# Kernel tuning notes

Hardware: AMD Instinct MI355X
Metric: run time of the kernel (lower is better)

The kernel has to match this reference:

```python
import jax, jax.numpy as jnp
import numpy as np

B, T = 2048, 256
VOCAB, E, H = 50000, 50, 50


def setup_inputs() -> dict:
    key = jax.random.key(0)
    ks = jax.random.split(key, 9)
    s = 0.1
    return {
        "batched_input": jax.random.randint(ks[0], (B, T), 0, VOCAB),
        "emb": jax.random.normal(ks[1], (VOCAB, E)) * s,
        "Wk": jax.random.normal(ks[2], (E, 4 * H)) * s,      # LSTM input kernel (i,f,c,o)
        "Uk": jax.random.normal(ks[3], (H, 4 * H)) * s,      # LSTM recurrent kernel
        "b": jnp.zeros((4 * H,)),                            # LSTM bias
        "W1": jax.random.normal(ks[4], (H, E)) * s,          # denseTypeOne (applied twice)
        "b1": jnp.zeros((E,)),
        "W2": jax.random.normal(ks[5], (E, 1)) * s,          # denseTypeTwo
        "b2": jnp.zeros((1,)),
    }


def _lstm(xg, Uk):
    # xg: [T, B, 4H] precomputed input projections; Keras gate order i,f,c,o
    Bsz = xg.shape[1]
    h0 = jnp.zeros((Bsz, H), xg.dtype)
    c0 = jnp.zeros((Bsz, H), xg.dtype)

    def step(carry, xt):
        h, c = carry
        z = xt + h @ Uk
        i, f, g, o = jnp.split(z, 4, axis=-1)
        i = jax.nn.sigmoid(i)
        f = jax.nn.sigmoid(f)
        g = jnp.tanh(g)
        o = jax.nn.sigmoid(o)
        c = f * c + i * g
        h = o * jnp.tanh(c)
        return (h, c), h

    (_, _), hs = jax.lax.scan(step, (h0, c0), xg)
    return hs  # [T, B, H]


def reference(batched_input, emb, Wk, Uk, b, W1, b1, W2, b2):
    x = emb[batched_input]                                  # [B, T, E]
    xg = jnp.einsum('bte,eg->tbg', x, Wk) + b               # [T, B, 4H]
    hs = _lstm(xg, Uk)                                      # [T, B, H]
    hs = jnp.transpose(hs, (1, 0, 2))                       # [B, T, H]
    d1 = jax.nn.relu(hs @ W1 + b1)                          # denseTypeOne
    d2 = jax.nn.relu(d1 @ W1 + b1)                          # denseTypeOne again (as in source)
    p = jax.nn.sigmoid(d2 @ W2 + b2)                        # [B, T, 1]
    return p.reshape(p.shape[0], -1)                        # Flatten -> [B, T]
```

## Files before the change

kernel.cpp:

```cpp
#include <hip/hip_runtime.h>


typedef unsigned short u16;
typedef unsigned int   u32;
typedef float f32x4 __attribute__((ext_vector_type(4)));
typedef short s16x8 __attribute__((ext_vector_type(8)));

__device__ __forceinline__ float bf2f(u16 u){
  union { u32 i; float f; } v; v.i = ((u32)u) << 16; return v.f;
}
__device__ __forceinline__ u16 f2bf(float f){
  union { float fl; u32 i; } v; v.fl = f;
  u32 r = v.i + 0x7fffu + ((v.i >> 16) & 1u);
  return (u16)(r >> 16);
}
__device__ __forceinline__ float frcp(float x){ return __builtin_amdgcn_rcpf(x); }
__device__ __forceinline__ float sigm_f(float x){
  float e = __expf(-x);
  return frcp(1.f + e);
}
__device__ __forceinline__ float tanh_f(float x){
  x = fminf(fmaxf(x, -15.f), 15.f);
  float e = __expf(-2.f * x);
  return (1.f - e) * frcp(1.f + e);
}
__device__ __forceinline__ f32x4 mf(s16x8 a, s16x8 b, f32x4 c){
  return __builtin_amdgcn_mfma_f32_16x16x32_bf16(a, b, c, 0, 0, 0);
}
__device__ __forceinline__ float ldf(const void* p, int i, bool f32in){
  if (f32in) return ((const float*)p)[i];
  return bf2f(((const u16*)p)[i]);
}

#define TPB 256
#define RPB 4

extern "C" __global__ __launch_bounds__(TPB, 2) void LSTM_Seq2Dis_15272903704706_kernel(
    const int* idx, const void* emb, const void* Wk, const void* Uk,
    const void* bias, const void* W1, const void* b1,
    const void* W2, const void* b2, float* out)
{
  __shared__ __align__(16) u16 ering[16][1024];
  __shared__ __align__(16) u16 abuf[2][1024];
  __shared__ __align__(16) u16 hbuf[4][2][512];
  __shared__ __align__(16) u16 dwork[4][2][512];
  __shared__ float zl[4*212];
  __shared__ float cl[4*52];
  __shared__ float bl[208];
  __shared__ int   tokl[1024];
  __shared__ int   s_f32;

  const int tid = threadIdx.x;
  const int wv  = tid >> 6, ln = tid & 63;
  const int r0  = blockIdx.x * RPB;

  if (tid == 0){
    const u32* ew = (const u32*)emb;
    int hits = 0;
    for (int i = 0; i < 64; i++){
      u32 ef = (ew[i] >> 7) & 0xFFu;
      if (ef >= 112u && ef <= 127u) hits++;
    }
    s_f32 = (hits < 32) ? 1 : 0;
  }

  for (int i = tid; i < 16*1024; i += TPB) ((u16*)ering)[i] = 0;
  for (int i = tid; i < 2*1024;  i += TPB) ((u16*)abuf)[i]  = 0;
  for (int i = tid; i < 4*2*512; i += TPB) ((u16*)hbuf)[i]  = 0;
  for (int i = tid; i < 4*52;    i += TPB) cl[i] = 0.f;
  for (int i = tid; i < 1024;    i += TPB){
    int r = i & 3, s = i >> 2;
    tokl[i] = idx[(r0 + r)*256 + s];
  }
  __syncthreads();
  const bool f32in = (s_f32 != 0);
  for (int i = tid; i < 208; i += TPB) bl[i] = (i < 200) ? ldf(bias, i, f32in) : 0.f;

  s16x8 bz[4][4];
  #pragma unroll
  for (int t = 0; t < 4; t++){
    int n = (wv + 4*t)*16 + (ln & 15);
    #pragma unroll
    for (int kt = 0; kt < 4; kt++){
      s16x8 v;
      #pragma unroll
      for (int j = 0; j < 8; j++){
        int k = kt*32 + ((ln >> 4) << 3) + j;
        float w = 0.f;
        if (n < 200){
          if (k < 50)                  w = ldf(Uk, k*200 + n, f32in);
          else if (k >= 64 && k < 114) w = ldf(Wk, (k-64)*200 + n, f32in);
        }
        v[j] = (short)f2bf(w);
      }
      bz[t][kt] = v;
    }
  }

  s16x8 w1f[4][2];
  float b1v[4], w2v[4];
  #pragma unroll
  for (int nt = 0; nt < 4; nt++){
    int c = nt*16 + (ln & 15);
    b1v[nt] = (c < 50) ? ldf(b1, c, f32in) : 0.f;
    w2v[nt] = (c < 50) ? ldf(W2, c, f32in) : 0.f;
    #pragma unroll
    for (int kt = 0; kt < 2; kt++){
      s16x8 v;
      #pragma unroll
      for (int j = 0; j < 8; j++){
        int k = kt*32 + ((ln >> 4) << 3) + j;
        v[j] = (short)((k < 50 && c < 50) ? f2bf(ldf(W1, k*50 + c, f32in)) : (u16)0);
      }
      w1f[nt][kt] = v;
    }
  }
  const float b2s = ldf(b2, 0, f32in);

  const int gr = tid / 50, gj = tid - gr*50;
  const int foff = (gj >> 5)*512 + (gr + (((gj & 31) >> 3) << 4))*8 + (gj & 7);
  __syncthreads();

  for (int ch = 0; ch < 16; ch++){
    const int tc = ch*16;

    if (tid < 200){
      float ev[16];
      #pragma unroll
      for (int sl = 0; sl < 16; sl++)
        ev[sl] = ldf(emb, tokl[(tc + sl)*4 + gr]*50 + gj, f32in);
      #pragma unroll
      for (int sl = 0; sl < 16; sl++)
        ering[sl][foff] = f2bf(ev[sl]);
    }
    __syncthreads();

    for (int sl = 0; sl < 16; sl++){
      const int s   = tc + sl;
      const int cur = s & 1, nxt = cur ^ 1;

      s16x8 av[4];
      av[0] = *(const s16x8*)&abuf[cur][ln*8];
      av[1] = *(const s16x8*)&abuf[cur][512 + ln*8];
      av[2] = *(const s16x8*)&ering[sl][ln*8];
      av[3] = *(const s16x8*)&ering[sl][512 + ln*8];
      #pragma unroll
      for (int t = 0; t < 4; t++){
        f32x4 acc = {0.f,0.f,0.f,0.f};
        #pragma unroll
        for (int kt = 0; kt < 4; kt++) acc = mf(av[kt], bz[t][kt], acc);
        if ((ln >> 4) == 0){
          int col = (wv + 4*t)*16 + (ln & 15);
          if (col < 200){
            #pragma unroll
            for (int r = 0; r < 4; r++) zl[r*212 + col] = acc[r];
          }
        }
      }
      __syncthreads();

      if (tid < 200){
        float zi = zl[gr*212 + gj]       + bl[gj];
        float zf = zl[gr*212 + 50 + gj]  + bl[50 + gj];
        float zg = zl[gr*212 + 100 + gj] + bl[100 + gj];
        float zo = zl[gr*212 + 150 + gj] + bl[150 + gj];
        float iv = sigm_f(zi), fv = sigm_f(zf), gv = tanh_f(zg), ov = sigm_f(zo);
        float c  = fv * cl[gr*52 + gj] + iv * gv;
        cl[gr*52 + gj] = c;
        u16 hb = f2bf(ov * tanh_f(c));
        abuf[nxt][foff] = hb;
        int m = sl*4 + gr;
        hbuf[m >> 4][gj >> 5][((m & 15) + (((gj & 31) >> 3) << 4))*8 + (gj & 7)] = hb;
      }

      if (sl == 15){
        __syncthreads();
        s16x8 a0 = *(const s16x8*)&hbuf[wv][0][ln*8];
        s16x8 a1 = *(const s16x8*)&hbuf[wv][1][ln*8];
        #pragma unroll
        for (int nt = 0; nt < 4; nt++){
          f32x4 acc = {0.f,0.f,0.f,0.f};
          acc = mf(a0, w1f[nt][0], acc);
          acc = mf(a1, w1f[nt][1], acc);
          int c = nt*16 + (ln & 15);
          #pragma unroll
          for (int r = 0; r < 4; r++){
            float v = fmaxf(acc[r] + b1v[nt], 0.f);
            int row16 = ((ln >> 4) << 2) + r;
            dwork[wv][c >> 5][(row16 + (((c & 31) >> 3) << 4))*8 + (c & 7)] = f2bf(v);
          }
        }
        s16x8 d0 = *(const s16x8*)&dwork[wv][0][ln*8];
        s16x8 d1 = *(const s16x8*)&dwork[wv][1][ln*8];
        float part[4] = {0.f,0.f,0.f,0.f};
        #pragma unroll
        for (int nt = 0; nt < 4; nt++){
          f32x4 acc = {0.f,0.f,0.f,0.f};
          acc = mf(d0, w1f[nt][0], acc);
          acc = mf(d1, w1f[nt][1], acc);
          #pragma unroll
          for (int r = 0; r < 4; r++)
            part[r] += fmaxf(acc[r] + b1v[nt], 0.f) * w2v[nt];
        }
        #pragma unroll
        for (int d = 1; d < 16; d <<= 1)
          #pragma unroll
          for (int r = 0; r < 4; r++) part[r] += __shfl_xor(part[r], d, 16);
        if ((ln & 15) == 0){
          int q = ln >> 4;
          #pragma unroll
          for (int r = 0; r < 4; r++){
            int m = wv*16 + (q << 2) + r;
            int sl4 = m >> 2, rb = m & 3;
            float z = part[r] + b2s;
            z = fmaxf(fminf(z, 1.0f), -1.0f);
            out[(r0 + rb)*256 + tc + sl4] = sigm_f(z);
          }
        }
      }
      __syncthreads();
    }
  }
}

extern "C" void kernel_launch(void* const* d_in, const int* in_sizes, int n_in,
                              void* d_out, int out_size, void* d_ws, size_t ws_size,
                              hipStream_t stream) {
  (void)in_sizes; (void)n_in; (void)out_size; (void)d_ws; (void)ws_size;
  hipLaunchKernelGGL(LSTM_Seq2Dis_15272903704706_kernel,
                     dim3(512), dim3(TPB), 0, stream,
                     (const int*)d_in[0], d_in[1], d_in[2], d_in[3], d_in[4],
                     d_in[5], d_in[6], d_in[7], d_in[8], (float*)d_out);
}
```

Before: 299.9 us.

## Precompute input-gate projections per chunk with batched MFMA, shorten recurrent step

Instead of folding the embedding-times-Wk product into every recurrent step's MFMA chain, the kernel now computes the input projections for all 16 timesteps of a chunk in one batched MFMA pass, adding the bias and storing the result as bf16 in shared memory. Each serial step then seeds its accumulator with that precomputed value and only multiplies by Uk. This halves the MFMA chain on the latency-bound recurrence. The cost is an extra bf16 rounding of the pre-activations and more shared memory.

```diff
diff --git a/kernel.cpp b/kernel.cpp
--- a/kernel.cpp
+++ b/kernel.cpp
@@ -40,7 +40,8 @@
     const void* bias, const void* W1, const void* b1,
     const void* W2, const void* b2, float* out)
 {
-  __shared__ __align__(16) u16 ering[16][1024];
+  __shared__ __align__(16) u16 ebuf[4][2][512];
+  __shared__ __align__(16) u16 xgl[16][4][212];
   __shared__ __align__(16) u16 abuf[2][1024];
   __shared__ __align__(16) u16 hbuf[4][2][512];
   __shared__ __align__(16) u16 dwork[4][2][512];
@@ -64,7 +65,7 @@
     s_f32 = (hits < 32) ? 1 : 0;
   }
 
-  for (int i = tid; i < 16*1024; i += TPB) ((u16*)ering)[i] = 0;
+  for (int i = tid; i < 4*2*512; i += TPB) ((u16*)ebuf)[i] = 0;
   for (int i = tid; i < 2*1024;  i += TPB) ((u16*)abuf)[i]  = 0;
   for (int i = tid; i < 4*2*512; i += TPB) ((u16*)hbuf)[i]  = 0;
   for (int i = tid; i < 4*52;    i += TPB) cl[i] = 0.f;
@@ -76,24 +77,25 @@
   const bool f32in = (s_f32 != 0);
   for (int i = tid; i < 208; i += TPB) bl[i] = (i < 200) ? ldf(bias, i, f32in) : 0.f;
 
-  s16x8 bz[4][4];
+  s16x8 ukf[4][2], wkf[4][2];
   #pragma unroll
   for (int t = 0; t < 4; t++){
-    int n = (wv + 4*t)*16 + (ln & 15);
+    const int n = (wv + 4*t)*16 + (ln & 15);
     #pragma unroll
-    for (int kt = 0; kt < 4; kt++){
-      s16x8 v;
+    for (int kt = 0; kt < 2; kt++){
+      s16x8 u, w;
       #pragma unroll
       for (int j = 0; j < 8; j++){
-        int k = kt*32 + ((ln >> 4) << 3) + j;
-        float w = 0.f;
-        if (n < 200){
-          if (k < 50)                  w = ldf(Uk, k*200 + n, f32in);
-          else if (k >= 64 && k < 114) w = ldf(Wk, (k-64)*200 + n, f32in);
-        }
-        v[j] = (short)f2bf(w);
-      }
-      bz[t][kt] = v;
+        const int k = kt*32 + ((ln >> 4) << 3) + j;
+        float uu = 0.f, ww = 0.f;
+        if (n < 200 && k < 50){
+          uu = ldf(Uk, k*200 + n, f32in);
+          ww = ldf(Wk, k*200 + n, f32in);
+        }
+        u[j] = (short)f2bf(uu);
+        w[j] = (short)f2bf(ww);
+      }
+      ukf[t][kt] = u; wkf[t][kt] = w;
     }
   }
 
@@ -129,9 +131,36 @@
       #pragma unroll
       for (int sl = 0; sl < 16; sl++)
         ev[sl] = ldf(emb, tokl[(tc + sl)*4 + gr]*50 + gj, f32in);
-      #pragma unroll
-      for (int sl = 0; sl < 16; sl++)
-        ering[sl][foff] = f2bf(ev[sl]);
+      const int kf = gj >> 5;
+      const int eo = ((gj & 31) >> 3) << 4;
+      const int jj = gj & 7;
+      #pragma unroll
+      for (int sl = 0; sl < 16; sl++){
+        const int m = sl*4 + gr;
+        ebuf[m >> 4][kf][(((m & 15) + eo) << 3) + jj] = f2bf(ev[sl]);
+      }
+    }
+    __syncthreads();
+
+    #pragma unroll
+    for (int mt = 0; mt < 4; mt++){
+      s16x8 e0 = *(const s16x8*)&ebuf[mt][0][ln*8];
+      s16x8 e1 = *(const s16x8*)&ebuf[mt][1][ln*8];
+      #pragma unroll
+      for (int t = 0; t < 4; t++){
+        f32x4 acc = {0.f,0.f,0.f,0.f};
+        acc = mf(e0, wkf[t][0], acc);
+        acc = mf(e1, wkf[t][1], acc);
+        const int col = (wv + 4*t)*16 + (ln & 15);
+        if (col < 200){
+          const float bv = bl[col];
+          #pragma unroll
+          for (int r = 0; r < 4; r++){
+            const int m = mt*16 + ((ln >> 4) << 2) + r;
+            xgl[m >> 2][m & 3][col] = f2bf(acc[r] + bv);
+          }
+        }
+      }
     }
     __syncthreads();
 
@@ -139,31 +168,31 @@
       const int s   = tc + sl;
       const int cur = s & 1, nxt = cur ^ 1;
 
-      s16x8 av[4];
-      av[0] = *(const s16x8*)&abuf[cur][ln*8];
-      av[1] = *(const s16x8*)&abuf[cur][512 + ln*8];
-      av[2] = *(const s16x8*)&ering[sl][ln*8];
-      av[3] = *(const s16x8*)&ering[sl][512 + ln*8];
+      s16x8 av0 = *(const s16x8*)&abuf[cur][ln*8];
+      s16x8 av1 = *(const s16x8*)&abuf[cur][512 + ln*8];
       #pragma unroll
       for (int t = 0; t < 4; t++){
+        const int col = (wv + 4*t)*16 + (ln & 15);
+        const bool wr = ((ln >> 4) == 0) && (col < 200);
         f32x4 acc = {0.f,0.f,0.f,0.f};
-        #pragma unroll
-        for (int kt = 0; kt < 4; kt++) acc = mf(av[kt], bz[t][kt], acc);
-        if ((ln >> 4) == 0){
-          int col = (wv + 4*t)*16 + (ln & 15);
-          if (col < 200){
-            #pragma unroll
-            for (int r = 0; r < 4; r++) zl[r*212 + col] = acc[r];
-          }
+        if (wr){
+          #pragma unroll
+          for (int r = 0; r < 4; r++) acc[r] = bf2f(xgl[sl][r][col]);
+        }
+        acc = mf(av0, ukf[t][0], acc);
+        acc = mf(av1, ukf[t][1], acc);
+        if (wr){
+          #pragma unroll
+          for (int r = 0; r < 4; r++) zl[r*212 + col] = acc[r];
         }
       }
       __syncthreads();
 
       if (tid < 200){
-        float zi = zl[gr*212 + gj]       + bl[gj];
-        float zf = zl[gr*212 + 50 + gj]  + bl[50 + gj];
-        float zg = zl[gr*212 + 100 + gj] + bl[100 + gj];
-        float zo = zl[gr*212 + 150 + gj] + bl[150 + gj];
+        float zi = zl[gr*212 + gj];
+        float zf = zl[gr*212 + 50 + gj];
+        float zg = zl[gr*212 + 100 + gj];
+        float zo = zl[gr*212 + 150 + gj];
         float iv = sigm_f(zi), fv = sigm_f(zf), gv = tanh_f(zg), ov = sigm_f(zo);
         float c  = fv * cl[gr*52 + gj] + iv * gv;
         cl[gr*52 + gj] = c;
```

Result: slower. 357.8 us (+19.3%).

## Process eight batch rows per block to fill more MFMA rows

Applied to the files above, without the earlier changes.

Doubles rows per block from 4 to 8 and halves the grid to 256 blocks with one block per CU. The recurrent MFMA now fills 8 of its 16 M rows instead of 4, so each MFMA call does twice the useful work. Each gate thread handles two rows, and each wave runs the dense head for two M tiles. The aim is to halve total recurrent MFMA and sync work, at the cost of fewer resident waves per CU to hide latency and a longer pointwise section inside each serial step.

```diff
diff --git a/kernel.cpp b/kernel.cpp
--- a/kernel.cpp
+++ b/kernel.cpp
@@ -33,21 +33,21 @@
 }
 
 #define TPB 256
-#define RPB 4
-
-extern "C" __global__ __launch_bounds__(TPB, 2) void LSTM_Seq2Dis_15272903704706_kernel(
+#define RPB 8
+
+extern "C" __global__ __launch_bounds__(TPB, 1) void LSTM_Seq2Dis_15272903704706_kernel(
     const int* idx, const void* emb, const void* Wk, const void* Uk,
     const void* bias, const void* W1, const void* b1,
     const void* W2, const void* b2, float* out)
 {
   __shared__ __align__(16) u16 ering[16][1024];
   __shared__ __align__(16) u16 abuf[2][1024];
-  __shared__ __align__(16) u16 hbuf[4][2][512];
+  __shared__ __align__(16) u16 hbuf[8][2][512];
   __shared__ __align__(16) u16 dwork[4][2][512];
-  __shared__ float zl[4*212];
-  __shared__ float cl[4*52];
+  __shared__ float zl[8*212];
+  __shared__ float cl[8*52];
   __shared__ float bl[208];
-  __shared__ int   tokl[1024];
+  __shared__ int   tokl[2048];
   __shared__ int   s_f32;
 
   const int tid = threadIdx.x;
@@ -66,10 +66,10 @@
 
   for (int i = tid; i < 16*1024; i += TPB) ((u16*)ering)[i] = 0;
   for (int i = tid; i < 2*1024;  i += TPB) ((u16*)abuf)[i]  = 0;
-  for (int i = tid; i < 4*2*512; i += TPB) ((u16*)hbuf)[i]  = 0;
-  for (int i = tid; i < 4*52;    i += TPB) cl[i] = 0.f;
-  for (int i = tid; i < 1024;    i += TPB){
-    int r = i & 3, s = i >> 2;
+  for (int i = tid; i < 8*2*512; i += TPB) ((u16*)hbuf)[i]  = 0;
+  for (int i = tid; i < 8*52;    i += TPB) cl[i] = 0.f;
+  for (int i = tid; i < 2048;    i += TPB){
+    int r = i & 7, s = i >> 3;
     tokl[i] = idx[(r0 + r)*256 + s];
   }
   __syncthreads();
@@ -128,10 +128,16 @@
       float ev[16];
       #pragma unroll
       for (int sl = 0; sl < 16; sl++)
-        ev[sl] = ldf(emb, tokl[(tc + sl)*4 + gr]*50 + gj, f32in);
+        ev[sl] = ldf(emb, tokl[(tc + sl)*8 + gr]*50 + gj, f32in);
       #pragma unroll
       for (int sl = 0; sl < 16; sl++)
         ering[sl][foff] = f2bf(ev[sl]);
+      #pragma unroll
+      for (int sl = 0; sl < 16; sl++)
+        ev[sl] = ldf(emb, tokl[(tc + sl)*8 + gr + 4]*50 + gj, f32in);
+      #pragma unroll
+      for (int sl = 0; sl < 16; sl++)
+        ering[sl][foff + 32] = f2bf(ev[sl]);
     }
     __syncthreads();
 
@@ -149,72 +155,81 @@
         f32x4 acc = {0.f,0.f,0.f,0.f};
         #pragma unroll
         for (int kt = 0; kt < 4; kt++) acc = mf(av[kt], bz[t][kt], acc);
-        if ((ln >> 4) == 0){
+        const int q = ln >> 4;
+        if (q < 2){
           int col = (wv + 4*t)*16 + (ln & 15);
           if (col < 200){
             #pragma unroll
-            for (int r = 0; r < 4; r++) zl[r*212 + col] = acc[r];
+            for (int r = 0; r < 4; r++) zl[(q*4 + r)*212 + col] = acc[r];
           }
         }
       }
       __syncthreads();
 
       if (tid < 200){
-        float zi = zl[gr*212 + gj]       + bl[gj];
-        float zf = zl[gr*212 + 50 + gj]  + bl[50 + gj];
-        float zg = zl[gr*212 + 100 + gj] + bl[100 + gj];
-        float zo = zl[gr*212 + 150 + gj] + bl[150 + gj];
-        float iv = sigm_f(zi), fv = sigm_f(zf), gv = tanh_f(zg), ov = sigm_f(zo);
-        float c  = fv * cl[gr*52 + gj] + iv * gv;
-        cl[gr*52 + gj] = c;
-        u16 hb = f2bf(ov * tanh_f(c));
-        abuf[nxt][foff] = hb;
-        int m = sl*4 + gr;
-        hbuf[m >> 4][gj >> 5][((m & 15) + (((gj & 31) >> 3) << 4))*8 + (gj & 7)] = hb;
+        #pragma unroll
+        for (int p = 0; p < 2; p++){
+          const int rr = gr + 4*p;
+          float zi = zl[rr*212 + gj]       + bl[gj];
+          float zf = zl[rr*212 + 50 + gj]  + bl[50 + gj];
+          float zg = zl[rr*212 + 100 + gj] + bl[100 + gj];
+          float zo = zl[rr*212 + 150 + gj] + bl[150 + gj];
+          float iv = sigm_f(zi), fv = sigm_f(zf), gv = tanh_f(zg), ov = sigm_f(zo);
+          float c  = fv * cl[rr*52 + gj] + iv * gv;
+          cl[rr*52 + gj] = c;
+          u16 hb = f2bf(ov * tanh_f(c));
+          abuf[nxt][foff + 32*p] = hb;
+          int m = sl*8 + rr;
+          hbuf[m >> 4][gj >> 5][((m & 15) + (((gj & 31) >> 3) << 4))*8 + (gj & 7)] = hb;
+        }
       }
 
       if (sl == 15){
         __syncthreads();
-        s16x8 a0 = *(const s16x8*)&hbuf[wv][0][ln*8];
-        s16x8 a1 = *(const s16x8*)&hbuf[wv][1][ln*8];
         #pragma unroll
-        for (int nt = 0; nt < 4; nt++){
-          f32x4 acc = {0.f,0.f,0.f,0.f};
-          acc = mf(a0, w1f[nt][0], acc);
-          acc = mf(a1, w1f[nt][1], acc);
-          int c = nt*16 + (ln & 15);
+        for (int p = 0; p < 2; p++){
+          const int mt = 2*wv + p;
+          s16x8 a0 = *(const s16x8*)&hbuf[mt][0][ln*8];
+          s16x8 a1 = *(const s16x8*)&hbuf[mt][1][ln*8];
           #pragma unroll
-          for (int r = 0; r < 4; r++){
-            float v = fmaxf(acc[r] + b1v[nt], 0.f);
-            int row16 = ((ln >> 4) << 2) + r;
-            dwork[wv][c >> 5][(row16 + (((c & 31) >> 3) << 4))*8 + (c & 7)] = f2bf(v);
-          }
-        }
-        s16x8 d0 = *(const s16x8*)&dwork[wv][0][ln*8];
-        s16x8 d1 = *(const s16x8*)&dwork[wv][1][ln*8];
-        float part[4] = {0.f,0.f,0.f,0.f};
-        #pragma unroll
-        for (int nt = 0; nt < 4; nt++){
-          f32x4 acc = {0.f,0.f,0.f,0.f};
-          acc = mf(d0, w1f[nt][0], acc);
-          acc = mf(d1, w1f[nt][1], acc);
+          for (int nt = 0; nt < 4; nt++){
+            f32x4 acc = {0.f,0.f,0.f,0.f};
+            acc = mf(a0, w1f[nt][0], acc);
+            acc = mf(a1, w1f[nt][1], acc);
+            int c = nt*16 + (ln & 15);
+            #pragma unroll
+            for (int r = 0; r < 4; r++){
+              float v = fmaxf(acc[r] + b1v[nt], 0.f);
+              int row16 = ((ln >> 4) << 2) + r;
+              dwork[wv][c >> 5][(row16 + (((c & 31) >> 3) << 4))*8 + (c & 7)] = f2bf(v);
+            }
+          }
+          s16x8 d0 = *(const s16x8*)&dwork[wv][0][ln*8];
+          s16x8 d1 = *(const s16x8*)&dwork[wv][1][ln*8];
+          float part[4] = {0.f,0.f,0.f,0.f};
           #pragma unroll
-          for (int r = 0; r < 4; r++)
-            part[r] += fmaxf(acc[r] + b1v[nt], 0.f) * w2v[nt];
-        }
-        #pragma unroll
-        for (int d = 1; d < 16; d <<= 1)
+          for (int nt = 0; nt < 4; nt++){
+            f32x4 acc = {0.f,0.f,0.f,0.f};
+            acc = mf(d0, w1f[nt][0], acc);
+            acc = mf(d1, w1f[nt][1], acc);
+            #pragma unroll
+            for (int r = 0; r < 4; r++)
+              part[r] += fmaxf(acc[r] + b1v[nt], 0.f) * w2v[nt];
+          }
           #pragma unroll
-          for (int r = 0; r < 4; r++) part[r] += __shfl_xor(part[r], d, 16);
-        if ((ln & 15) == 0){
-          int q = ln >> 4;
-          #pragma unroll
-          for (int r = 0; r < 4; r++){
-            int m = wv*16 + (q << 2) + r;
-            int sl4 = m >> 2, rb = m & 3;
-            float z = part[r] + b2s;
-            z = fmaxf(fminf(z, 1.0f), -1.0f);
-            out[(r0 + rb)*256 + tc + sl4] = sigm_f(z);
+          for (int d = 1; d < 16; d <<= 1)
+            #pragma unroll
+            for (int r = 0; r < 4; r++) part[r] += __shfl_xor(part[r], d, 16);
+          if ((ln & 15) == 0){
+            int q = ln >> 4;
+            #pragma unroll
+            for (int r = 0; r < 4; r++){
+              int m = mt*16 + (q << 2) + r;
+              int sl8 = m >> 3, rb = m & 7;
+              float z = part[r] + b2s;
+              z = fmaxf(fminf(z, 1.0f), -1.0f);
+              out[(r0 + rb)*256 + tc + sl8] = sigm_f(z);
+            }
           }
         }
       }
@@ -228,7 +243,7 @@
                               hipStream_t stream) {
   (void)in_sizes; (void)n_in; (void)out_size; (void)d_ws; (void)ws_size;
   hipLaunchKernelGGL(LSTM_Seq2Dis_15272903704706_kernel,
-                     dim3(512), dim3(TPB), 0, stream,
+                     dim3(256), dim3(TPB), 0, stream,
                      (const int*)d_in[0], d_in[1], d_in[2], d_in[3], d_in[4],
                      d_in[5], d_in[6], d_in[7], d_in[8], (float*)d_out);
 }
```

After: 362.0 us. +20.7%, slower.
